# Performance work log

Measured on AMD Instinct MI355X. Metric: run time of the kernel, lower is better.

## Reference

```python
import jax, jax.numpy as jnp
import numpy as np

CC = 16  # content_channels
NODES = [128, 512, 2048, 8192, 32768, 65536]  # level sizes, coarse->fine
CH_IN = [128 + CC, 64 + CC, 32 + CC, 16 + CC, 8 + CC]
CH_OUT = [64, 32, 16, 8, 1]


def _wn(v, g):
    # torch weight_norm(dim=0) on an [num, cc] embedding: per-row renormalize
    return g * v / jnp.linalg.norm(v, axis=1, keepdims=True)


def setup_inputs() -> dict:
    key = jax.random.key(0)
    ks = iter(jax.random.split(key, 64))
    B = 64
    inp = {}
    inp['z'] = jax.random.normal(next(ks), (B, 128), dtype=jnp.float32)
    inp['studies'] = jax.random.randint(next(ks), (B,), 0, 10)
    inp['tasks'] = jax.random.randint(next(ks), (B,), 0, 50)
    inp['contrasts'] = jax.random.randint(next(ks), (B,), 0, 200)
    # one parent per fine node (ward-tree upsampling adjacency, transposed)
    for i in range(5):
        inp[f'p{i}'] = jax.random.randint(next(ks), (NODES[i + 1],), 0, NODES[i], dtype=jnp.int32)
    # weight-normed embeddings: direction v + gain g
    for name, n in (('s', 10), ('t', 50), ('c', 200)):
        inp[f'emb_{name}_v'] = jax.random.normal(next(ks), (n, CC), dtype=jnp.float32)
        inp[f'emb_{name}_g'] = jnp.ones((n, 1), dtype=jnp.float32)
    # content FCs: Linear(i_cc*CC -> CC), i_cc in [1,2,3,3,3]
    for i, mult in enumerate([1, 2, 3, 3, 3]):
        fan = mult * CC
        inp[f'fc{i}_w'] = jax.random.normal(next(ks), (fan, CC), dtype=jnp.float32) / np.sqrt(fan)
        inp[f'fc{i}_b'] = jnp.zeros((CC,), dtype=jnp.float32)
    # FGL layer weights
    for i in range(5):
        inp[f'W{i}'] = jax.random.normal(next(ks), (CH_IN[i], CH_OUT[i]), dtype=jnp.float32) / np.sqrt(CH_IN[i])
        inp[f'b{i}'] = jnp.zeros((CH_OUT[i],), dtype=jnp.float32)
    return inp


def reference(z, studies, tasks, contrasts, p0, p1, p2, p3, p4,
              emb_s_v, emb_s_g, emb_t_v, emb_t_g, emb_c_v, emb_c_g,
              fc0_w, fc0_b, fc1_w, fc1_b, fc2_w, fc2_b, fc3_w, fc3_b, fc4_w, fc4_b,
              W0, b0, W1, b1, W2, b2, W3, b3, W4, b4):
    B = z.shape[0]
    se = _wn(emb_s_v, emb_s_g)[studies]          # [B, CC]
    te = _wn(emb_t_v, emb_t_g)[tasks]
    ce = _wn(emb_c_v, emb_c_g)[contrasts]
    cat2 = jnp.concatenate([se, te], axis=1)
    cat3 = jnp.concatenate([se, te, ce], axis=1)
    # dropout is identity at eval time
    contents = [se @ fc0_w + fc0_b,
                cat2 @ fc1_w + fc1_b,
                cat3 @ fc2_w + fc2_b,
                cat3 @ fc3_w + fc3_b,
                cat3 @ fc4_w + fc4_b]            # each [B, CC]
    Ws = [W0, W1, W2, W3, W4]
    bs = [b0, b1, b2, b3, b4]
    ps = [p0, p1, p2, p3, p4]
    cur = jnp.broadcast_to(z[:, None, :], (B, NODES[0], z.shape[1]))  # [B,128,128]
    for i in range(5):
        n_in = cur.shape[1]
        c = jnp.broadcast_to(contents[i][:, None, :], (B, n_in, CC))
        x = jnp.concatenate([cur, c], axis=2)          # [B, n_in, ch_in]
        h = jnp.einsum('bnc,cd->bnd', x, Ws[i])        # dense per-node linear
        cur = h[:, ps[i], :] + bs[i]                   # sparse upsample = gather
        if i < 4:
            cur = jax.nn.leaky_relu(cur, 0.2)
    return cur  # [B, n_leaves, 1]
```

## Files before the change

kernel.cpp:

```cpp
#include <hip/hip_runtime.h>
#include <hip/hip_bf16.h>


template <int F>
__device__ __forceinline__ float LDF(const void* p, int i) {
    if (F) return ((const float*)p)[i];
    return __bfloat162float(((const __hip_bfloat16*)p)[i]);
}
template <int I>
__device__ __forceinline__ int IDXT(const void* p, int i) {
    if (I) return (int)((const long long*)p)[i];
    return ((const int*)p)[i];
}

struct ChainArgs {
    const void *z, *studies, *tasks, *contrasts;
    const void *emb_s_v, *emb_s_g, *emb_t_v, *emb_t_g, *emb_c_v, *emb_c_g;
    const void *fc_w[5], *fc_b[5];
    const void *W[5], *bias[5];
};

struct Smem {
    float cat3[48];
    float contents[80];
    float xa[160];
    float xb[96];
    float partial[256];
    float res;
};

__device__ __forceinline__ float lrelu(float a) { return fmaxf(a, 0.2f * a); }

template <int F, int I>
__device__ __forceinline__ void chain_fill(
    const ChainArgs& a, float* __restrict__ out, int b, int slice, int t, Smem& sm)
{
    float zr = 0.f;
    if (t >= 48 && t < 176) zr = LDF<F>(a.z, b * 128 + (t - 48));

    int row = 0;
    if (t < 48) {
        const int g = t >> 4;
        if (g == 0)      row = IDXT<I>(a.studies, b);
        else if (g == 1) row = IDXT<I>(a.tasks, b);
        else             row = IDXT<I>(a.contrasts, b);
    }

    float w0r[36];
    {   const int j = t & 63, q = t >> 6;
        #pragma unroll
        for (int k = 0; k < 36; ++k) w0r[k] = LDF<F>(a.W[0], (q * 36 + k) * 64 + j);
    }
    float w1r[10];
    {   const int j = t & 31, q = t >> 5;
        #pragma unroll
        for (int k = 0; k < 10; ++k) w1r[k] = LDF<F>(a.W[1], (q * 10 + k) * 32 + j);
    }
    float w2r[3];
    {   const int j = t & 15, q = t >> 4;
        #pragma unroll
        for (int k = 0; k < 3; ++k) w2r[k] = LDF<F>(a.W[2], (q * 3 + k) * 16 + j);
    }
    float w3r;
    {   const int j = t & 7, q = t >> 3;
        w3r = LDF<F>(a.W[3], q * 8 + j);
    }
    float w4r = (t < 24) ? LDF<F>(a.W[4], t) : 0.f;
    float b0r = (t < 64) ? LDF<F>(a.bias[0], t) : 0.f;
    float b1r = (t < 32) ? LDF<F>(a.bias[1], t) : 0.f;
    float b2r = (t < 16) ? LDF<F>(a.bias[2], t) : 0.f;
    float b3r = (t < 8)  ? LDF<F>(a.bias[3], t) : 0.f;
    float b4r = (t == 0) ? LDF<F>(a.bias[4], 0) : 0.f;

    float fcw[48];
    float fcb = 0.f;
    if (t < 16) {
        fcb = LDF<F>(a.fc_b[0], t);
        #pragma unroll
        for (int k = 0; k < 16; ++k) fcw[k] = LDF<F>(a.fc_w[0], k * 16 + t);
    } else if (t < 32) {
        const int j = t & 15;
        fcb = LDF<F>(a.fc_b[1], j);
        #pragma unroll
        for (int k = 0; k < 32; ++k) fcw[k] = LDF<F>(a.fc_w[1], k * 16 + j);
    } else if (t < 48) {
        const int j = t & 15;
        fcb = LDF<F>(a.fc_b[2], j);
        #pragma unroll
        for (int k = 0; k < 48; ++k) fcw[k] = LDF<F>(a.fc_w[2], k * 16 + j);
    } else if (t < 64) {
        const int j = t & 15;
        fcb = LDF<F>(a.fc_b[3], j);
        #pragma unroll
        for (int k = 0; k < 48; ++k) fcw[k] = LDF<F>(a.fc_w[3], k * 16 + j);
    } else if (t < 80) {
        const int j = t & 15;
        fcb = LDF<F>(a.fc_b[4], j);
        #pragma unroll
        for (int k = 0; k < 48; ++k) fcw[k] = LDF<F>(a.fc_w[4], k * 16 + j);
    }

    if (t < 48) {
        const int g = t >> 4, j = t & 15;
        const void* v  = (g == 0) ? a.emb_s_v : (g == 1) ? a.emb_t_v : a.emb_c_v;
        const void* gp = (g == 0) ? a.emb_s_g : (g == 1) ? a.emb_t_g : a.emb_c_g;
        float gain = LDF<F>(gp, row);
        float vr[16];
        #pragma unroll
        for (int k = 0; k < 16; ++k) vr[k] = LDF<F>(v, row * 16 + k);
        float n2 = 0.f;
        #pragma unroll
        for (int k = 0; k < 16; ++k) n2 += vr[k] * vr[k];
        sm.cat3[t] = gain * vr[j] * rsqrtf(n2);
    } else if (t < 176) {
        sm.xa[t - 48] = zr;
    }
    __syncthreads();

    if (t < 16) {
        float acc = fcb;
        #pragma unroll
        for (int k = 0; k < 16; ++k) acc += sm.cat3[k] * fcw[k];
        sm.xa[128 + t] = acc;
    } else if (t < 32) {
        const int j = t & 15;
        float acc = fcb;
        #pragma unroll
        for (int k = 0; k < 32; ++k) acc += sm.cat3[k] * fcw[k];
        sm.contents[16 + j] = acc;
    } else if (t < 80) {
        const int i = t >> 4, j = t & 15;
        float acc = fcb;
        #pragma unroll
        for (int k = 0; k < 48; ++k) acc += sm.cat3[k] * fcw[k];
        sm.contents[i * 16 + j] = acc;
    }
    __syncthreads();

    {
        const int q = t >> 6;
        float acc = 0.f;
        #pragma unroll
        for (int k = 0; k < 36; ++k) acc += sm.xa[q * 36 + k] * w0r[k];
        sm.partial[t] = acc;
    }
    __syncthreads();
    if (t < 64) {
        float acc = b0r + sm.partial[t] + sm.partial[64 + t] + sm.partial[128 + t] + sm.partial[192 + t];
        sm.xb[t] = lrelu(acc);
    } else if (t < 80) {
        sm.xb[t] = sm.contents[16 + (t - 64)];
    }
    __syncthreads();

    {
        const int q = t >> 5;
        float acc = 0.f;
        #pragma unroll
        for (int k = 0; k < 10; ++k) acc += sm.xb[q * 10 + k] * w1r[k];
        sm.partial[t] = acc;
    }
    __syncthreads();
    if (t < 32) {
        float acc = b1r;
        #pragma unroll
        for (int q = 0; q < 8; ++q) acc += sm.partial[q * 32 + t];
        sm.xa[t] = lrelu(acc);
    } else if (t < 48) {
        sm.xa[t] = sm.contents[32 + (t - 32)];
    }
    __syncthreads();

    {
        const int q = t >> 4;
        float acc = 0.f;
        #pragma unroll
        for (int k = 0; k < 3; ++k) acc += sm.xa[q * 3 + k] * w2r[k];
        sm.partial[t] = acc;
    }
    __syncthreads();
    if (t < 16) {
        float acc = b2r;
        #pragma unroll
        for (int q = 0; q < 16; ++q) acc += sm.partial[q * 16 + t];
        sm.xb[t] = lrelu(acc);
    } else if (t < 32) {
        sm.xb[t] = sm.contents[48 + (t - 16)];
    }
    __syncthreads();

    {
        const int q = t >> 3;
        sm.partial[t] = sm.xb[q] * w3r;
    }
    __syncthreads();
    if (t < 8) {
        float acc = b3r;
        #pragma unroll
        for (int q = 0; q < 32; ++q) acc += sm.partial[q * 8 + t];
        sm.xa[t] = lrelu(acc);
    } else if (t < 24) {
        sm.xa[t] = sm.contents[64 + (t - 8)];
    }
    __syncthreads();

    if (t < 24) sm.partial[t] = sm.xa[t] * w4r;
    __syncthreads();
    if (t == 0) {
        float acc = b4r;
        #pragma unroll
        for (int k = 0; k < 24; ++k) acc += sm.partial[k];
        sm.res = acc;
    }
    __syncthreads();

    const float v = sm.res;
    const float4 val = make_float4(v, v, v, v);
    float4* __restrict__ o = reinterpret_cast<float4*>(out) + (size_t)b * 16384 + slice * 2048;
    #pragma unroll
    for (int k = 0; k < 8; ++k) o[k * 256 + t] = val;
}

__global__ __launch_bounds__(256) void fgl_fused_kernel(ChainArgs a, float* __restrict__ out)
{
    const int b = blockIdx.x >> 3;
    const int slice = blockIdx.x & 7;
    const int t = threadIdx.x;

    __shared__ Smem sm;
    __shared__ int FI_s;

    if (t < 64) {
        bool fcond = false, icond = false;
        if (t < 32) {
            unsigned int wz = ((const unsigned int*)a.z)[t];
            fcond = ((wz >> 7) & 0xFF) >= 0x89;
            icond = (((const unsigned int*)a.contrasts)[2 * t + 1] != 0u);
        }
        unsigned long long bf = __ballot(fcond);
        unsigned long long bi = __ballot(icond);
        if (t == 0) FI_s = (bf ? 1 : 0) | ((bi == 0ull) ? 2 : 0);
    }
    __syncthreads();
    const int FI = FI_s;

    if (FI == 1)      chain_fill<1, 0>(a, out, b, slice, t, sm);
    else if (FI == 3) chain_fill<1, 1>(a, out, b, slice, t, sm);
    else if (FI == 0) chain_fill<0, 0>(a, out, b, slice, t, sm);
    else              chain_fill<0, 1>(a, out, b, slice, t, sm);
}

extern "C" void kernel_launch(void* const* d_in, const int* in_sizes, int n_in,
                              void* d_out, int out_size, void* d_ws, size_t ws_size,
                              hipStream_t stream) {
    ChainArgs a;
    a.z = d_in[0];
    a.studies = d_in[1];
    a.tasks = d_in[2];
    a.contrasts = d_in[3];
    a.emb_s_v = d_in[9];  a.emb_s_g = d_in[10];
    a.emb_t_v = d_in[11]; a.emb_t_g = d_in[12];
    a.emb_c_v = d_in[13]; a.emb_c_g = d_in[14];
    for (int i = 0; i < 5; ++i) {
        a.fc_w[i] = d_in[15 + 2 * i];
        a.fc_b[i] = d_in[16 + 2 * i];
        a.W[i]    = d_in[25 + 2 * i];
        a.bias[i] = d_in[26 + 2 * i];
    }
    fgl_fused_kernel<<<512, 256, 0, stream>>>(a, (float*)d_out);
}
```

Before: 13.97 us.

## Replace shared-memory partial reductions with wave-shuffle matvecs for layers 1-4

After layer 0, each wavefront now runs the small layer 1-4 matvecs by itself. Hidden activations are broadcast across lanes with __shfl, and weights are read directly from global memory. This drops the many block-wide __syncthreads and shared-memory partial-sum stages between the tiny layers. The per-thread register preloads of the layer 1-4 and FC weights are removed and those loads now happen inline, which may expose load latency on the serial chain. Every wave computes the same result redundantly, trading extra ALU and cache traffic for fewer barriers.

```diff
diff --git a/kernel.cpp b/kernel.cpp
--- a/kernel.cpp
+++ b/kernel.cpp
@@ -23,10 +23,8 @@
 struct Smem {
     float cat3[48];
     float contents[80];
-    float xa[160];
-    float xb[96];
+    float xa[144];
     float partial[256];
-    float res;
 };
 
 __device__ __forceinline__ float lrelu(float a) { return fmaxf(a, 0.2f * a); }
@@ -35,73 +33,19 @@
 __device__ __forceinline__ void chain_fill(
     const ChainArgs& a, float* __restrict__ out, int b, int slice, int t, Smem& sm)
 {
-    float zr = 0.f;
-    if (t >= 48 && t < 176) zr = LDF<F>(a.z, b * 128 + (t - 48));
+    const int lane = t & 63;
+    const int q    = t >> 6;
 
-    int row = 0;
+    float w0r[36];
+    #pragma unroll
+    for (int k = 0; k < 36; ++k) w0r[k] = LDF<F>(a.W[0], (q * 36 + k) * 64 + lane);
+
     if (t < 48) {
-        const int g = t >> 4;
+        const int g = t >> 4, j = t & 15;
+        int row;
         if (g == 0)      row = IDXT<I>(a.studies, b);
         else if (g == 1) row = IDXT<I>(a.tasks, b);
         else             row = IDXT<I>(a.contrasts, b);
-    }
-
-    float w0r[36];
-    {   const int j = t & 63, q = t >> 6;
-        #pragma unroll
-        for (int k = 0; k < 36; ++k) w0r[k] = LDF<F>(a.W[0], (q * 36 + k) * 64 + j);
-    }
-    float w1r[10];
-    {   const int j = t & 31, q = t >> 5;
-        #pragma unroll
-        for (int k = 0; k < 10; ++k) w1r[k] = LDF<F>(a.W[1], (q * 10 + k) * 32 + j);
-    }
-    float w2r[3];
-    {   const int j = t & 15, q = t >> 4;
-        #pragma unroll
-        for (int k = 0; k < 3; ++k) w2r[k] = LDF<F>(a.W[2], (q * 3 + k) * 16 + j);
-    }
-    float w3r;
-    {   const int j = t & 7, q = t >> 3;
-        w3r = LDF<F>(a.W[3], q * 8 + j);
-    }
-    float w4r = (t < 24) ? LDF<F>(a.W[4], t) : 0.f;
-    float b0r = (t < 64) ? LDF<F>(a.bias[0], t) : 0.f;
-    float b1r = (t < 32) ? LDF<F>(a.bias[1], t) : 0.f;
-    float b2r = (t < 16) ? LDF<F>(a.bias[2], t) : 0.f;
-    float b3r = (t < 8)  ? LDF<F>(a.bias[3], t) : 0.f;
-    float b4r = (t == 0) ? LDF<F>(a.bias[4], 0) : 0.f;
-
-    float fcw[48];
-    float fcb = 0.f;
-    if (t < 16) {
-        fcb = LDF<F>(a.fc_b[0], t);
-        #pragma unroll
-        for (int k = 0; k < 16; ++k) fcw[k] = LDF<F>(a.fc_w[0], k * 16 + t);
-    } else if (t < 32) {
-        const int j = t & 15;
-        fcb = LDF<F>(a.fc_b[1], j);
-        #pragma unroll
-        for (int k = 0; k < 32; ++k) fcw[k] = LDF<F>(a.fc_w[1], k * 16 + j);
-    } else if (t < 48) {
-        const int j = t & 15;
-        fcb = LDF<F>(a.fc_b[2], j);
-        #pragma unroll
-        for (int k = 0; k < 48; ++k) fcw[k] = LDF<F>(a.fc_w[2], k * 16 + j);
-    } else if (t < 64) {
-        const int j = t & 15;
-        fcb = LDF<F>(a.fc_b[3], j);
-        #pragma unroll
-        for (int k = 0; k < 48; ++k) fcw[k] = LDF<F>(a.fc_w[3], k * 16 + j);
-    } else if (t < 80) {
-        const int j = t & 15;
-        fcb = LDF<F>(a.fc_b[4], j);
-        #pragma unroll
-        for (int k = 0; k < 48; ++k) fcw[k] = LDF<F>(a.fc_w[4], k * 16 + j);
-    }
-
-    if (t < 48) {
-        const int g = t >> 4, j = t & 15;
         const void* v  = (g == 0) ? a.emb_s_v : (g == 1) ? a.emb_t_v : a.emb_c_v;
         const void* gp = (g == 0) ? a.emb_s_g : (g == 1) ? a.emb_t_g : a.emb_c_g;
         float gain = LDF<F>(gp, row);
@@ -113,109 +57,87 @@
         for (int k = 0; k < 16; ++k) n2 += vr[k] * vr[k];
         sm.cat3[t] = gain * vr[j] * rsqrtf(n2);
     } else if (t < 176) {
-        sm.xa[t - 48] = zr;
+        sm.xa[t - 48] = LDF<F>(a.z, b * 128 + (t - 48));
     }
     __syncthreads();
 
     if (t < 16) {
-        float acc = fcb;
+        float acc = LDF<F>(a.fc_b[0], t);
         #pragma unroll
-        for (int k = 0; k < 16; ++k) acc += sm.cat3[k] * fcw[k];
+        for (int k = 0; k < 16; ++k) acc += sm.cat3[k] * LDF<F>(a.fc_w[0], k * 16 + t);
         sm.xa[128 + t] = acc;
     } else if (t < 32) {
         const int j = t & 15;
-        float acc = fcb;
+        float acc = LDF<F>(a.fc_b[1], j);
         #pragma unroll
-        for (int k = 0; k < 32; ++k) acc += sm.cat3[k] * fcw[k];
+        for (int k = 0; k < 32; ++k) acc += sm.cat3[k] * LDF<F>(a.fc_w[1], k * 16 + j);
         sm.contents[16 + j] = acc;
     } else if (t < 80) {
         const int i = t >> 4, j = t & 15;
-        float acc = fcb;
+        const void* fw = a.fc_w[i];
+        float acc = LDF<F>(a.fc_b[i], j);
         #pragma unroll
-        for (int k = 0; k < 48; ++k) acc += sm.cat3[k] * fcw[k];
+        for (int k = 0; k < 48; ++k) acc += sm.cat3[k] * LDF<F>(fw, k * 16 + j);
         sm.contents[i * 16 + j] = acc;
     }
     __syncthreads();
 
     {
-        const int q = t >> 6;
         float acc = 0.f;
         #pragma unroll
         for (int k = 0; k < 36; ++k) acc += sm.xa[q * 36 + k] * w0r[k];
         sm.partial[t] = acc;
     }
     __syncthreads();
-    if (t < 64) {
-        float acc = b0r + sm.partial[t] + sm.partial[64 + t] + sm.partial[128 + t] + sm.partial[192 + t];
-        sm.xb[t] = lrelu(acc);
-    } else if (t < 80) {
-        sm.xb[t] = sm.contents[16 + (t - 64)];
+
+    float h0 = lrelu(LDF<F>(a.bias[0], lane)
+                     + sm.partial[lane] + sm.partial[64 + lane]
+                     + sm.partial[128 + lane] + sm.partial[192 + lane]);
+
+    float h1;
+    {
+        const int j = lane & 31;
+        float acc = LDF<F>(a.bias[1], j);
+        #pragma unroll
+        for (int k = 0; k < 64; ++k) acc += __shfl(h0, k) * LDF<F>(a.W[1], k * 32 + j);
+        #pragma unroll
+        for (int k = 0; k < 16; ++k) acc += sm.contents[16 + k] * LDF<F>(a.W[1], (64 + k) * 32 + j);
+        h1 = lrelu(acc);
     }
-    __syncthreads();
 
+    float h2;
     {
-        const int q = t >> 5;
-        float acc = 0.f;
+        const int j = lane & 15;
+        float acc = LDF<F>(a.bias[2], j);
         #pragma unroll
-        for (int k = 0; k < 10; ++k) acc += sm.xb[q * 10 + k] * w1r[k];
-        sm.partial[t] = acc;
+        for (int k = 0; k < 32; ++k) acc += __shfl(h1, k) * LDF<F>(a.W[2], k * 16 + j);
+        #pragma unroll
+        for (int k = 0; k < 16; ++k) acc += sm.contents[32 + k] * LDF<F>(a.W[2], (32 + k) * 16 + j);
+        h2 = lrelu(acc);
     }
-    __syncthreads();
-    if (t < 32) {
-        float acc = b1r;
+
+    float h3;
+    {
+        const int j = lane & 7;
+        float acc = LDF<F>(a.bias[3], j);
         #pragma unroll
-        for (int q = 0; q < 8; ++q) acc += sm.partial[q * 32 + t];
-        sm.xa[t] = lrelu(acc);
-    } else if (t < 48) {
-        sm.xa[t] = sm.contents[32 + (t - 32)];
+        for (int k = 0; k < 16; ++k) acc += __shfl(h2, k) * LDF<F>(a.W[3], k * 8 + j);
+        #pragma unroll
+        for (int k = 0; k < 16; ++k) acc += sm.contents[48 + k] * LDF<F>(a.W[3], (16 + k) * 8 + j);
+        h3 = lrelu(acc);
     }
-    __syncthreads();
 
+    float res;
     {
-        const int q = t >> 4;
-        float acc = 0.f;
+        float acc = LDF<F>(a.bias[4], 0);
         #pragma unroll
-        for (int k = 0; k < 3; ++k) acc += sm.xa[q * 3 + k] * w2r[k];
-        sm.partial[t] = acc;
+        for (int k = 0; k < 8; ++k)  acc += __shfl(h3, k) * LDF<F>(a.W[4], k);
+        #pragma unroll
+        for (int k = 0; k < 16; ++k) acc += sm.contents[64 + k] * LDF<F>(a.W[4], 8 + k);
+        res = acc;
     }
-    __syncthreads();
-    if (t < 16) {
-        float acc = b2r;
-        #pragma unroll
-        for (int q = 0; q < 16; ++q) acc += sm.partial[q * 16 + t];
-        sm.xb[t] = lrelu(acc);
-    } else if (t < 32) {
-        sm.xb[t] = sm.contents[48 + (t - 16)];
-    }
-    __syncthreads();
 
-    {
-        const int q = t >> 3;
-        sm.partial[t] = sm.xb[q] * w3r;
-    }
-    __syncthreads();
-    if (t < 8) {
-        float acc = b3r;
-        #pragma unroll
-        for (int q = 0; q < 32; ++q) acc += sm.partial[q * 8 + t];
-        sm.xa[t] = lrelu(acc);
-    } else if (t < 24) {
-        sm.xa[t] = sm.contents[64 + (t - 8)];
-    }
-    __syncthreads();
-
-    if (t < 24) sm.partial[t] = sm.xa[t] * w4r;
-    __syncthreads();
-    if (t == 0) {
-        float acc = b4r;
-        #pragma unroll
-        for (int k = 0; k < 24; ++k) acc += sm.partial[k];
-        sm.res = acc;
-    }
-    __syncthreads();
-
-    const float v = sm.res;
-    const float4 val = make_float4(v, v, v, v);
+    const float4 val = make_float4(res, res, res, res);
     float4* __restrict__ o = reinterpret_cast<float4*>(out) + (size_t)b * 16384 + slice * 2048;
     #pragma unroll
     for (int k = 0; k < 8; ++k) o[k * 256 + t] = val;
@@ -244,10 +166,11 @@
     __syncthreads();
     const int FI = FI_s;
 
-    if (FI == 1)      chain_fill<1, 0>(a, out, b, slice, t, sm);
-    else if (FI == 3) chain_fill<1, 1>(a, out, b, slice, t, sm);
-    else if (FI == 0) chain_fill<0, 0>(a, out, b, slice, t, sm);
-    else              chain_fill<0, 1>(a, out, b, slice, t, sm);
+    if (FI == 1)      chain_fill<1, 0>(a, out, b >> 0, blockIdx.x & 7, t, sm);
+    else if (FI == 3) chain_fill<1, 1>(a, out, b, blockIdx.x & 7, t, sm);
+    else if (FI == 0) chain_fill<0, 0>(a, out, b, blockIdx.x & 7, t, sm);
+    else              chain_fill<0, 1>(a, out, b, blockIdx.x & 7, t, sm);
+    (void)slice;
 }
 
 extern "C" void kernel_launch(void* const* d_in, const int* in_sizes, int n_in,
```

After: 18.02 us. +29.0%, slower.
